# Performance work log

Measured on AMD Instinct MI355X. Metric: run time of the kernel, lower is better.

The kernel has to match this reference:

```python
import jax, jax.numpy as jnp
import numpy as np

B, SQ, SK, D_MODEL, H, D = 2, 2048, 2048, 1024, 16, 64


def setup_inputs() -> dict:
    key = jax.random.key(0)
    ks = jax.random.split(key, 10)
    s = 1.0 / np.sqrt(D_MODEL)
    return {
        "x": jax.random.normal(ks[0], (B, SK, D_MODEL), jnp.float32),
        "x2": jax.random.normal(ks[1], (B, SQ, D_MODEL), jnp.float32),
        "Wq": jax.random.normal(ks[2], (H, D_MODEL, D), jnp.float32) * s,
        "bq": jax.random.normal(ks[3], (H, D), jnp.float32) * s,
        "Wk": jax.random.normal(ks[4], (H, D_MODEL, D), jnp.float32) * s,
        "bk": jax.random.normal(ks[5], (H, D), jnp.float32) * s,
        "Wv": jax.random.normal(ks[6], (H, D_MODEL, D), jnp.float32) * s,
        "bv": jax.random.normal(ks[7], (H, D), jnp.float32) * s,
        "Wo": jax.random.normal(ks[8], (D_MODEL, D_MODEL), jnp.float32) * s,
        "bo": jax.random.normal(ks[9], (D_MODEL,), jnp.float32) * s,
    }


def reference(x, x2, Wq, bq, Wk, bk, Wv, bv, Wo, bo):
    # Batched per-head projections (fuses the Python per-head loop).
    # q: [B, H, SQ, D]; k,v: [B, H, SK, D]
    q = jnp.einsum("bsm,hmd->bhsd", x2, Wq) + bq[None, :, None, :]
    k = jnp.einsum("bsm,hmd->bhsd", x, Wk) + bk[None, :, None, :]
    v = jnp.einsum("bsm,hmd->bhsd", x, Wv) + bv[None, :, None, :]
    scale = 1.0 / jnp.sqrt(jnp.asarray(D, q.dtype))
    scores = jnp.einsum("bhqd,bhkd->bhqk", q, k) * scale  # [B,H,SQ,SK]
    attn = jax.nn.softmax(scores, axis=-1)
    o = jnp.einsum("bhqk,bhkd->bhqd", attn, v)  # [B,H,SQ,D]
    # concat heads along feature dim (head-major order matches torch.cat)
    o = o.transpose(0, 2, 1, 3).reshape(B, SQ, H * D)
    # final projection; dropout is identity in eval mode
    return o @ Wo.T + bo
```

## Files before the change

### kernel.cpp

```cpp
#include <hip/hip_runtime.h>
#include <math.h>

#define B_   2
#define SQ_  2048
#define SK_  2048
#define DM_  1024
#define H_   16
#define D_   64

typedef __attribute__((ext_vector_type(8))) short bf16x8;
typedef __attribute__((ext_vector_type(4))) float f32x4;
typedef unsigned int u32;

__device__ __forceinline__ short f2bf(float f) {
    union { float f; unsigned u; } v; v.f = f;
    unsigned r = v.u + 0x7FFFu + ((v.u >> 16) & 1u);
    return (short)(r >> 16);
}
__device__ __forceinline__ u32 pk2bf(float x, float y) {
    union { float f; u32 u; } a, b; a.f = x; b.f = y;
    return ((a.u + 0x8000u) >> 16) | ((b.u + 0x8000u) & 0xFFFF0000u);
}
__device__ __forceinline__ u32 pkbf_rh(float x, float y) {
    union { float f; u32 u; } a, b; a.f = x; b.f = y;
    return __builtin_amdgcn_perm(b.u + 0x8000u, a.u + 0x8000u, 0x07060302u);
}

__device__ __forceinline__ void gll16(const void* g, void* l) {
    __builtin_amdgcn_global_load_lds(
        (const __attribute__((address_space(1))) u32*)g,
        (__attribute__((address_space(3))) u32*)l, 16, 0, 0);
}

__global__ __launch_bounds__(256) void prep_kernel(
    const float* __restrict__ Wq, const float* __restrict__ Wk,
    const float* __restrict__ Wv, const float* __restrict__ Wo,
    const float* __restrict__ x,  const float* __restrict__ x2,
    short* __restrict__ WqT, short* __restrict__ WkT,
    short* __restrict__ WvT, short* __restrict__ Wob,
    short* __restrict__ xb,  short* __restrict__ x2b)
{
    const int t = threadIdx.x;
    const int z = blockIdx.z;
    if (z >= 3) {
        const float* src = (z == 3) ? Wo : (z == 4) ? x : x2;
        short* dst       = (z == 3) ? Wob : (z == 4) ? xb : x2b;
        int nloop = (z == 3) ? 4 : 16;
        int bid = blockIdx.y * 16 + blockIdx.x;
        #pragma unroll 4
        for (int j = 0; j < nloop; j++) {
            int i = bid * (nloop * 256) + j * 256 + t;
            float4 v = ((const float4*)src)[i];
            short4 s;
            s.x = f2bf(v.x); s.y = f2bf(v.y); s.z = f2bf(v.z); s.w = f2bf(v.w);
            ((short4*)dst)[i] = s;
        }
        return;
    }
    const float* W = (z == 0) ? Wq : (z == 1) ? Wk : Wv;
    short* WT      = (z == 0) ? WqT : (z == 1) ? WkT : WvT;
    const int h  = blockIdx.y;
    const int m0 = blockIdx.x * 64;
    __shared__ short Ls[64][68];

    #pragma unroll
    for (int it = 0; it < 4; it++) {
        int lin = it * 256 + t;
        int m = lin >> 4, d4 = lin & 15;
        float4 v = *(const float4*)&W[((long)h * DM_ + m0 + m) * D_ + d4 * 4];
        short4 s;
        s.x = f2bf(v.x); s.y = f2bf(v.y); s.z = f2bf(v.z); s.w = f2bf(v.w);
        *(short4*)&Ls[m][d4 * 4] = s;
    }
    __syncthreads();
    #pragma unroll
    for (int it = 0; it < 2; it++) {
        int d = (t >> 3) + it * 32, scol = t & 7;
        bf16x8 vv;
        #pragma unroll
        for (int j = 0; j < 8; j++) vv[j] = Ls[scol * 8 + j][d];
        *(bf16x8*)&WT[((long)h * 64 + d) * DM_ + m0 + scol * 8] = vv;
    }
}

__device__ __forceinline__ void gemm_stage(
    short* __restrict__ Asb, short* __restrict__ Bsb,
    const short* __restrict__ A, const short* __restrict__ Bw,
    int r0, int n0, int k0c, int w, int srow, int sc)
{
    #pragma unroll
    for (int j = 0; j < 4; j++) {
        int q   = w * 4 + j;
        int row = q * 8 + srow;
        gll16(A  + ((long)(r0 + row) << 10) + k0c + sc * 8, Asb + q * 512);
        gll16(Bw + ((long)(n0 + row) << 10) + k0c + sc * 8, Bsb + q * 512);
    }
}

template <int MODE>
__device__ __forceinline__ void gemm_core(
    short* __restrict__ Ls,
    const short* __restrict__ A, const short* __restrict__ Bw,
    const float* __restrict__ bias, void* __restrict__ outp,
    int r0, int n0, float oscale)
{
    const int t    = threadIdx.x;
    const int w    = t >> 6;
    const int ln   = t & 63;
    const int l15  = ln & 15;
    const int quad = ln >> 4;
    const int wr   = w >> 1;
    const int wc   = w & 1;

    f32x4 acc[4][4];
    #pragma unroll
    for (int i = 0; i < 4; i++)
        #pragma unroll
        for (int j = 0; j < 4; j++) acc[i][j] = (f32x4){0.f, 0.f, 0.f, 0.f};

    const int srow = ln >> 3;
    const int sc   = (ln & 7) ^ srow;
    const int rsw  = l15 & 7;

    gemm_stage(Ls, Ls + 8192, A, Bw, r0, n0, 0, w, srow, sc);

    int cur = 0;
    for (int k0 = 0; k0 < 1024; k0 += 64) {
        __syncthreads();
        if (k0 + 64 < 1024) {
            short* Anx = Ls + (cur ^ 1) * 16384;
            gemm_stage(Anx, Anx + 8192, A, Bw, r0, n0, k0 + 64, w, srow, sc);
        }
        const short* Asb = Ls + cur * 16384;
        const short* Bsb = Asb + 8192;
        #pragma unroll
        for (int kh = 0; kh < 2; kh++) {
            bf16x8 af[4], bfr[4];
            #pragma unroll
            for (int i = 0; i < 4; i++) {
                int ra = wr * 64 + i * 16 + l15;
                int rb = wc * 64 + i * 16 + l15;
                int pc = ((kh * 4 + quad) ^ rsw) * 8;
                af[i]  = *(const bf16x8*)&Asb[ra * 64 + pc];
                bfr[i] = *(const bf16x8*)&Bsb[rb * 64 + pc];
            }
            #pragma unroll
            for (int i = 0; i < 4; i++)
                #pragma unroll
                for (int j = 0; j < 4; j++)
                    acc[i][j] = __builtin_amdgcn_mfma_f32_16x16x32_bf16(
                        af[i], bfr[j], acc[i][j], 0, 0, 0);
        }
        cur ^= 1;
    }

    #pragma unroll
    for (int j = 0; j < 4; j++) {
        int col = n0 + wc * 64 + j * 16 + l15;
        float bv = bias[col];
        if (MODE == 2) {
            int hh = col >> 6, dd = col & 63;
            #pragma unroll
            for (int i = 0; i < 4; i++) {
                int rowb = r0 + wr * 64 + i * 16 + quad * 4;
                int bb = rowb >> 11, ss = rowb & 2047;
                int sl = ss & 63;
                int sp = (ss & ~63) | (sl & 35) | ((sl & 12) << 1) | ((sl & 16) >> 2);
                short4 sv;
                sv.x = f2bf(acc[i][j][0] + bv);
                sv.y = f2bf(acc[i][j][1] + bv);
                sv.z = f2bf(acc[i][j][2] + bv);
                sv.w = f2bf(acc[i][j][3] + bv);
                *(short4*)&((short*)outp)[
                    ((long)(((bb << 4) + hh) * 64 + dd) << 11) + sp] = sv;
            }
        } else {
            #pragma unroll
            for (int i = 0; i < 4; i++) {
                int rowb = r0 + wr * 64 + i * 16 + quad * 4;
                #pragma unroll
                for (int r = 0; r < 4; r++) {
                    float v = (acc[i][j][r] + bv) * oscale;
                    if (MODE == 0)
                        ((short*)outp)[(long)(rowb + r) * 1024 + col] = f2bf(v);
                    else
                        ((float*)outp)[(long)(rowb + r) * 1024 + col] = v;
                }
            }
        }
    }
}

#define QSCALE 0.180336880977f

__global__ __launch_bounds__(256) void gemm_qkv_kernel(
    const short* __restrict__ x2b, const short* __restrict__ xb,
    const short* __restrict__ WqT, const short* __restrict__ WkT,
    const short* __restrict__ WvT,
    const float* __restrict__ bq, const float* __restrict__ bk,
    const float* __restrict__ bv,
    short* __restrict__ Qb, short* __restrict__ Kb, short* __restrict__ VT)
{
    __shared__ short Ls[2 * 16384];
    const int z = blockIdx.z;
    if (z == 0) {
        gemm_core<0>(Ls, x2b, WqT, bq, Qb, blockIdx.x * 128, blockIdx.y * 128, QSCALE);
    } else if (z == 1) {
        gemm_core<0>(Ls, xb, WkT, bk, Kb, blockIdx.x * 128, blockIdx.y * 128, 1.0f);
    } else {
        gemm_core<2>(Ls, xb, WvT, bv, VT, blockIdx.x * 128, blockIdx.y * 128, 1.0f);
    }
}

__device__ __forceinline__ void gout_stage(
    short* __restrict__ Asb, short* __restrict__ Bsb,
    const short* __restrict__ A, const short* __restrict__ Bw,
    int r0, int n0, int k0c, int w, int srow, int sc)
{
    #pragma unroll
    for (int j = 0; j < 6; j++) {
        int q = w * 6 + j;
        if (q < 8) {
            int row = q * 8 + srow;
            gll16(A + ((long)(r0 + row) << 10) + k0c + sc * 8, Asb + q * 512);
        } else {
            int qb = q - 8;
            int row = qb * 8 + srow;
            gll16(Bw + ((long)(n0 + row) << 10) + k0c + sc * 8, Bsb + qb * 512);
        }
    }
}

__global__ __launch_bounds__(256) void gemm_out_kernel(
    const short* __restrict__ A, const short* __restrict__ Bw,
    const float* __restrict__ bias, float* __restrict__ outp)
{
    __shared__ short Ls[2 * 12288];

    const int r0   = blockIdx.x * 64;
    const int n0   = blockIdx.y * 128;
    const int t    = threadIdx.x;
    const int w    = t >> 6;
    const int ln   = t & 63;
    const int l15  = ln & 15;
    const int quad = ln >> 4;
    const int wr   = w >> 1;
    const int wc   = w & 1;

    f32x4 acc[2][4];
    #pragma unroll
    for (int i = 0; i < 2; i++)
        #pragma unroll
        for (int j = 0; j < 4; j++) acc[i][j] = (f32x4){0.f, 0.f, 0.f, 0.f};

    const int srow = ln >> 3;
    const int sc   = (ln & 7) ^ srow;
    const int rsw  = l15 & 7;

    gout_stage(Ls, Ls + 4096, A, Bw, r0, n0, 0, w, srow, sc);

    int cur = 0;
    for (int k0 = 0; k0 < 1024; k0 += 64) {
        __syncthreads();
        if (k0 + 64 < 1024) {
            short* Anx = Ls + (cur ^ 1) * 12288;
            gout_stage(Anx, Anx + 4096, A, Bw, r0, n0, k0 + 64, w, srow, sc);
        }
        const short* Asb = Ls + cur * 12288;
        const short* Bsb = Asb + 4096;
        #pragma unroll
        for (int kh = 0; kh < 2; kh++) {
            int pc = ((kh * 4 + quad) ^ rsw) * 8;
            bf16x8 af[2], bfr[4];
            #pragma unroll
            for (int i = 0; i < 2; i++)
                af[i] = *(const bf16x8*)&Asb[(wr * 32 + i * 16 + l15) * 64 + pc];
            #pragma unroll
            for (int j = 0; j < 4; j++)
                bfr[j] = *(const bf16x8*)&Bsb[(wc * 64 + j * 16 + l15) * 64 + pc];
            #pragma unroll
            for (int i = 0; i < 2; i++)
                #pragma unroll
                for (int j = 0; j < 4; j++)
                    acc[i][j] = __builtin_amdgcn_mfma_f32_16x16x32_bf16(
                        af[i], bfr[j], acc[i][j], 0, 0, 0);
        }
        cur ^= 1;
    }

    #pragma unroll
    for (int j = 0; j < 4; j++) {
        int col = n0 + wc * 64 + j * 16 + l15;
        float bv = bias[col];
        #pragma unroll
        for (int i = 0; i < 2; i++) {
            int rowb = r0 + wr * 32 + i * 16 + quad * 4;
            #pragma unroll
            for (int r = 0; r < 4; r++)
                outp[(long)(rowb + r) * 1024 + col] = acc[i][j][r] + bv;
        }
    }
}

__global__ __launch_bounds__(256, 2) void flash_kernel(
    const short* __restrict__ Q, const short* __restrict__ K,
    const short* __restrict__ VT, short* __restrict__ O)
{
    const int t    = threadIdx.x;
    const int wave = t >> 6;
    const int ln   = t & 63;
    const int l15  = ln & 15;
    const int quad = ln >> 4;
    const int f   = blockIdx.x + (blockIdx.y << 4);
    const int wid = ((f & 7) << 6) | (f >> 3);
    const int bh  = wid >> 4;
    const int b   = bh >> 4;
    const int h   = bh & 15;
    const int q0  = (wid & 15) * 128;
    const int wq  = q0 + wave * 32;

    __shared__ short Ks[2][2][64 * 64];
    __shared__ short Vs[2][2][64 * 64];

    const int srow = ln >> 3;
    const int sc   = (ln & 7) ^ srow;
    const int rsw  = l15 & 7;
    const int pc0  = ((quad    ) ^ rsw) * 8;
    const int pc1  = ((quad + 4) ^ rsw) * 8;
    const int rb   = l15 * 64;

    bf16x8 aQ0[2], aQ1[2];
    #pragma unroll
    for (int qg = 0; qg < 2; qg++) {
        const short* Qp = Q + ((long)(b * SQ_ + wq + qg * 16 + l15)) * 1024
                            + h * 64 + quad * 8;
        aQ0[qg] = *(const bf16x8*)(Qp);
        aQ1[qg] = *(const bf16x8*)(Qp + 32);
    }

    bf16x8 ones;
    #pragma unroll
    for (int j = 0; j < 8; j++) ones[j] = (short)0x3F80;

    const f32x4 fz = (f32x4){0.f, 0.f, 0.f, 0.f};

    f32x4 o_acc[2][4];
    f32x4 l_acc[2];
    #pragma unroll
    for (int qg = 0; qg < 2; qg++) {
        l_acc[qg] = fz;
        #pragma unroll
        for (int i = 0; i < 4; i++) o_acc[qg][i] = fz;
    }

    const short* Kbase = K  + ((long)b * SK_) * 1024 + h * 64;
    const short* Vbase = VT + (long)bh * D_ * SK_;
    const int qqa = wave * 2, qqb = wave * 2 + 1;
    const int rowa = qqa * 8 + srow, rowb_ = qqb * 8 + srow;

    #define STAGE(bufp, half, kbase)                                            \
        gll16(Kbase + (long)((kbase) + rowa)  * 1024 + sc * 8,                  \
              &Ks[bufp][half][qqa * 512]);                                      \
        gll16(Kbase + (long)((kbase) + rowb_) * 1024 + sc * 8,                  \
              &Ks[bufp][half][qqb * 512]);                                      \
        gll16(Vbase + (long)rowa  * 2048 + (kbase) + sc * 8,                    \
              &Vs[bufp][half][qqa * 512]);                                      \
        gll16(Vbase + (long)rowb_ * 2048 + (kbase) + sc * 8,                    \
              &Vs[bufp][half][qqb * 512]);

    STAGE(0, 0, 0)
    STAGE(0, 1, 64)

    u32 pwB[2][8];
    bf16x8 vfB[8];

    int cur = 0;
    for (int k0 = 0; k0 < SK_; k0 += 128) {
        __syncthreads();
        if (k0 + 128 < SK_) {
            int nx = cur ^ 1;
            STAGE(nx, 0, k0 + 128)
            STAGE(nx, 1, k0 + 192)
        }
        const short* K0 = &Ks[cur][0][0];
        const short* K1 = &Ks[cur][1][0];
        const short* V0 = &Vs[cur][0][0];
        const short* V1 = &Vs[cur][1][0];

        bf16x8 kfA[8];
        #pragma unroll
        for (int kt = 0; kt < 4; kt++) {
            const short* kr = &K0[kt * 1024 + rb];
            kfA[kt * 2    ] = *(const bf16x8*)&kr[pc0];
            kfA[kt * 2 + 1] = *(const bf16x8*)&kr[pc1];
        }

        if (k0) {
            bf16x8 aP0B[2], aP1B[2];
            #pragma unroll
            for (int qg = 0; qg < 2; qg++) {
                union { bf16x8 v; u32 w[4]; } u0, u1;
                u0.w[0] = pwB[qg][0]; u0.w[1] = pwB[qg][1];
                u0.w[2] = pwB[qg][2]; u0.w[3] = pwB[qg][3];
                u1.w[0] = pwB[qg][4]; u1.w[1] = pwB[qg][5];
                u1.w[2] = pwB[qg][6]; u1.w[3] = pwB[qg][7];
                aP0B[qg] = u0.v; aP1B[qg] = u1.v;
            }
            __builtin_amdgcn_s_setprio(1);
            #pragma unroll
            for (int qg = 0; qg < 2; qg++) {
                l_acc[qg] = __builtin_amdgcn_mfma_f32_16x16x32_bf16(aP0B[qg], ones, l_acc[qg], 0, 0, 0);
                l_acc[qg] = __builtin_amdgcn_mfma_f32_16x16x32_bf16(aP1B[qg], ones, l_acc[qg], 0, 0, 0);
            }
            #pragma unroll
            for (int dt = 0; dt < 4; dt++) {
                #pragma unroll
                for (int qg = 0; qg < 2; qg++) {
                    o_acc[qg][dt] = __builtin_amdgcn_mfma_f32_16x16x32_bf16(aP0B[qg], vfB[dt * 2    ], o_acc[qg][dt], 0, 0, 0);
                    o_acc[qg][dt] = __builtin_amdgcn_mfma_f32_16x16x32_bf16(aP1B[qg], vfB[dt * 2 + 1], o_acc[qg][dt], 0, 0, 0);
                }
            }
            __builtin_amdgcn_s_setprio(0);
        }

        bf16x8 kfB[8];
        #pragma unroll
        for (int kt = 0; kt < 4; kt++) {
            const short* kr = &K1[kt * 1024 + rb];
            kfB[kt * 2    ] = *(const bf16x8*)&kr[pc0];
            kfB[kt * 2 + 1] = *(const bf16x8*)&kr[pc1];
        }
        f32x4 zA[2][4], zB[2][4];
        #pragma unroll
        for (int kt = 0; kt < 4; kt++)
            #pragma unroll
            for (int qg = 0; qg < 2; qg++) {
                f32x4 z = __builtin_amdgcn_mfma_f32_16x16x32_bf16(kfA[kt * 2], aQ0[qg], fz, 0, 0, 0);
                zA[qg][kt] = __builtin_amdgcn_mfma_f32_16x16x32_bf16(kfA[kt * 2 + 1], aQ1[qg], z, 0, 0, 0);
            }

        bf16x8 vfA[8];
        #pragma unroll
        for (int dt = 0; dt < 4; dt++) {
            const short* vr = &V0[dt * 1024 + rb];
            vfA[dt * 2    ] = *(const bf16x8*)&vr[pc0];
            vfA[dt * 2 + 1] = *(const bf16x8*)&vr[pc1];
        }
        u32 pwA[2][8];
        #pragma unroll
        for (int kt = 0; kt < 4; kt++) {
            #pragma unroll
            for (int qg = 0; qg < 2; qg++) {
                f32x4 z = __builtin_amdgcn_mfma_f32_16x16x32_bf16(kfB[kt * 2], aQ0[qg], fz, 0, 0, 0);
                zB[qg][kt] = __builtin_amdgcn_mfma_f32_16x16x32_bf16(kfB[kt * 2 + 1], aQ1[qg], z, 0, 0, 0);
            }
            #pragma unroll
            for (int qg = 0; qg < 2; qg++) {
                f32x4 s = zA[qg][kt];
                pwA[qg][kt * 2    ] = pkbf_rh(__builtin_amdgcn_exp2f(s[0]),
                                              __builtin_amdgcn_exp2f(s[1]));
                pwA[qg][kt * 2 + 1] = pkbf_rh(__builtin_amdgcn_exp2f(s[2]),
                                              __builtin_amdgcn_exp2f(s[3]));
            }
        }

        bf16x8 aP0A[2], aP1A[2];
        #pragma unroll
        for (int qg = 0; qg < 2; qg++) {
            union { bf16x8 v; u32 w[4]; } u0, u1;
            u0.w[0] = pwA[qg][0]; u0.w[1] = pwA[qg][1];
            u0.w[2] = pwA[qg][2]; u0.w[3] = pwA[qg][3];
            u1.w[0] = pwA[qg][4]; u1.w[1] = pwA[qg][5];
            u1.w[2] = pwA[qg][6]; u1.w[3] = pwA[qg][7];
            aP0A[qg] = u0.v; aP1A[qg] = u1.v;
            l_acc[qg] = __builtin_amdgcn_mfma_f32_16x16x32_bf16(aP0A[qg], ones, l_acc[qg], 0, 0, 0);
            l_acc[qg] = __builtin_amdgcn_mfma_f32_16x16x32_bf16(aP1A[qg], ones, l_acc[qg], 0, 0, 0);
        }

        #pragma unroll
        for (int dt = 0; dt < 4; dt++) {
            const short* vr = &V1[dt * 1024 + rb];
            vfB[dt * 2    ] = *(const bf16x8*)&vr[pc0];
            vfB[dt * 2 + 1] = *(const bf16x8*)&vr[pc1];
        }
        #pragma unroll
        for (int dt = 0; dt < 4; dt++) {
            #pragma unroll
            for (int qg = 0; qg < 2; qg++) {
                o_acc[qg][dt] = __builtin_amdgcn_mfma_f32_16x16x32_bf16(aP0A[qg], vfA[dt * 2    ], o_acc[qg][dt], 0, 0, 0);
                o_acc[qg][dt] = __builtin_amdgcn_mfma_f32_16x16x32_bf16(aP1A[qg], vfA[dt * 2 + 1], o_acc[qg][dt], 0, 0, 0);
            }
            #pragma unroll
            for (int qg = 0; qg < 2; qg++) {
                f32x4 s = zB[qg][dt];
                pwB[qg][dt * 2    ] = pkbf_rh(__builtin_amdgcn_exp2f(s[0]),
                                              __builtin_amdgcn_exp2f(s[1]));
                pwB[qg][dt * 2 + 1] = pkbf_rh(__builtin_amdgcn_exp2f(s[2]),
                                              __builtin_amdgcn_exp2f(s[3]));
            }
        }
        cur ^= 1;
    }
    #undef STAGE

    {
        bf16x8 aP0B[2], aP1B[2];
        #pragma unroll
        for (int qg = 0; qg < 2; qg++) {
            union { bf16x8 v; u32 w[4]; } u0, u1;
            u0.w[0] = pwB[qg][0]; u0.w[1] = pwB[qg][1];
            u0.w[2] = pwB[qg][2]; u0.w[3] = pwB[qg][3];
            u1.w[0] = pwB[qg][4]; u1.w[1] = pwB[qg][5];
            u1.w[2] = pwB[qg][6]; u1.w[3] = pwB[qg][7];
            aP0B[qg] = u0.v; aP1B[qg] = u1.v;
            l_acc[qg] = __builtin_amdgcn_mfma_f32_16x16x32_bf16(aP0B[qg], ones, l_acc[qg], 0, 0, 0);
            l_acc[qg] = __builtin_amdgcn_mfma_f32_16x16x32_bf16(aP1B[qg], ones, l_acc[qg], 0, 0, 0);
        }
        #pragma unroll
        for (int dt = 0; dt < 4; dt++) {
            #pragma unroll
            for (int qg = 0; qg < 2; qg++) {
                o_acc[qg][dt] = __builtin_amdgcn_mfma_f32_16x16x32_bf16(aP0B[qg], vfB[dt * 2    ], o_acc[qg][dt], 0, 0, 0);
                o_acc[qg][dt] = __builtin_amdgcn_mfma_f32_16x16x32_bf16(aP1B[qg], vfB[dt * 2 + 1], o_acc[qg][dt], 0, 0, 0);
            }
        }
    }

    #pragma unroll
    for (int qg = 0; qg < 2; qg++) {
        #pragma unroll
        for (int r = 0; r < 4; r++) {
            float inv = 1.0f / l_acc[qg][r];
            long row = (long)b * SQ_ + wq + qg * 16 + quad * 4 + r;
            short* Op = O + row * 1024 + h * 64 + l15;
            #pragma unroll
            for (int dt = 0; dt < 4; dt++)
                Op[dt * 16] = f2bf(o_acc[qg][dt][r] * inv);
        }
    }
}

extern "C" void kernel_launch(void* const* d_in, const int* in_sizes, int n_in,
                              void* d_out, int out_size, void* d_ws, size_t ws_size,
                              hipStream_t stream) {
    const float* x  = (const float*)d_in[0];
    const float* x2 = (const float*)d_in[1];
    const float* Wq = (const float*)d_in[2];
    const float* bq = (const float*)d_in[3];
    const float* Wk = (const float*)d_in[4];
    const float* bk = (const float*)d_in[5];
    const float* Wv = (const float*)d_in[6];
    const float* bv = (const float*)d_in[7];
    const float* Wo = (const float*)d_in[8];
    const float* bo = (const float*)d_in[9];
    float* out = (float*)d_out;

    const size_t nAct = (size_t)B_ * SK_ * DM_;
    const size_t nW   = (size_t)DM_ * DM_;
    short* bufA = (short*)d_ws;
    short* bufB = bufA + nAct;
    short* Qb   = bufB + nAct;
    short* Kb   = Qb + nAct;
    short* VTws = Kb + nAct;
    short* WqT  = VTws + nAct;
    short* WkT  = WqT + nW;
    short* WvT  = WkT + nW;
    short* Wob  = WvT + nW;

    prep_kernel<<<dim3(16, 16, 6), 256, 0, stream>>>(
        Wq, Wk, Wv, Wo, x, x2, WqT, WkT, WvT, Wob, bufA, bufB);

    gemm_qkv_kernel<<<dim3(32, 8, 3), 256, 0, stream>>>(
        bufB, bufA, WqT, WkT, WvT, bq, bk, bv, Qb, Kb, VTws);

    flash_kernel<<<dim3(16, 32), 256, 0, stream>>>(Qb, Kb, VTws, bufB);
    gemm_out_kernel<<<dim3(64, 8), 256, 0, stream>>>(bufB, Wob, bo, out);
}
```

Before: 190.3 us.

## Give each flash-attention wave 64 query rows with 2-wave blocks

Each flash kernel block now uses 2 waves (128 threads) instead of 4, and each wave processes 64 query rows (4 groups of 16) instead of 32. Every K/V fragment read from LDS is therefore reused across twice as many query rows, which lowers LDS read traffic per MFMA, and staging is split across fewer waves with four loads each. The cost is much higher register pressure from doubled accumulators, score tiles and P words. With launch bounds of 1 block per CU that could cut occupancy or cause spills, and fewer waves remain to hide latency.

```diff
diff --git a/kernel.cpp b/kernel.cpp
--- a/kernel.cpp
+++ b/kernel.cpp
@@ -302,7 +302,8 @@
     }
 }
 
-__global__ __launch_bounds__(256, 2) void flash_kernel(
+#define QG 4
+__global__ __launch_bounds__(128, 1) void flash_kernel(
     const short* __restrict__ Q, const short* __restrict__ K,
     const short* __restrict__ VT, short* __restrict__ O)
 {
@@ -317,7 +318,7 @@
     const int b   = bh >> 4;
     const int h   = bh & 15;
     const int q0  = (wid & 15) * 128;
-    const int wq  = q0 + wave * 32;
+    const int wq  = q0 + wave * 64;
 
     __shared__ short Ks[2][2][64 * 64];
     __shared__ short Vs[2][2][64 * 64];
@@ -329,9 +330,9 @@
     const int pc1  = ((quad + 4) ^ rsw) * 8;
     const int rb   = l15 * 64;
 
-    bf16x8 aQ0[2], aQ1[2];
-    #pragma unroll
-    for (int qg = 0; qg < 2; qg++) {
+    bf16x8 aQ0[QG], aQ1[QG];
+    #pragma unroll
+    for (int qg = 0; qg < QG; qg++) {
         const short* Qp = Q + ((long)(b * SQ_ + wq + qg * 16 + l15)) * 1024
                             + h * 64 + quad * 8;
         aQ0[qg] = *(const bf16x8*)(Qp);
@@ -344,10 +345,10 @@
 
     const f32x4 fz = (f32x4){0.f, 0.f, 0.f, 0.f};
 
-    f32x4 o_acc[2][4];
-    f32x4 l_acc[2];
-    #pragma unroll
-    for (int qg = 0; qg < 2; qg++) {
+    f32x4 o_acc[QG][4];
+    f32x4 l_acc[QG];
+    #pragma unroll
+    for (int qg = 0; qg < QG; qg++) {
         l_acc[qg] = fz;
         #pragma unroll
         for (int i = 0; i < 4; i++) o_acc[qg][i] = fz;
@@ -355,23 +356,22 @@
 
     const short* Kbase = K  + ((long)b * SK_) * 1024 + h * 64;
     const short* Vbase = VT + (long)bh * D_ * SK_;
-    const int qqa = wave * 2, qqb = wave * 2 + 1;
-    const int rowa = qqa * 8 + srow, rowb_ = qqb * 8 + srow;
 
     #define STAGE(bufp, half, kbase)                                            \
-        gll16(Kbase + (long)((kbase) + rowa)  * 1024 + sc * 8,                  \
-              &Ks[bufp][half][qqa * 512]);                                      \
-        gll16(Kbase + (long)((kbase) + rowb_) * 1024 + sc * 8,                  \
-              &Ks[bufp][half][qqb * 512]);                                      \
-        gll16(Vbase + (long)rowa  * 2048 + (kbase) + sc * 8,                    \
-              &Vs[bufp][half][qqa * 512]);                                      \
-        gll16(Vbase + (long)rowb_ * 2048 + (kbase) + sc * 8,                    \
-              &Vs[bufp][half][qqb * 512]);
+        _Pragma("unroll")                                                       \
+        for (int j_ = 0; j_ < 4; j_++) {                                        \
+            int qq_  = wave * 4 + j_;                                           \
+            int row_ = qq_ * 8 + srow;                                          \
+            gll16(Kbase + (long)((kbase) + row_) * 1024 + sc * 8,               \
+                  &Ks[bufp][half][qq_ * 512]);                                  \
+            gll16(Vbase + (long)row_ * 2048 + (kbase) + sc * 8,                 \
+                  &Vs[bufp][half][qq_ * 512]);                                  \
+        }
 
     STAGE(0, 0, 0)
     STAGE(0, 1, 64)
 
-    u32 pwB[2][8];
+    u32 pwB[QG][8];
     bf16x8 vfB[8];
 
     int cur = 0;
@@ -396,28 +396,20 @@
         }
 
         if (k0) {
-            bf16x8 aP0B[2], aP1B[2];
-            #pragma unroll
-            for (int qg = 0; qg < 2; qg++) {
+            __builtin_amdgcn_s_setprio(1);
+            #pragma unroll
+            for (int qg = 0; qg < QG; qg++) {
                 union { bf16x8 v; u32 w[4]; } u0, u1;
                 u0.w[0] = pwB[qg][0]; u0.w[1] = pwB[qg][1];
                 u0.w[2] = pwB[qg][2]; u0.w[3] = pwB[qg][3];
                 u1.w[0] = pwB[qg][4]; u1.w[1] = pwB[qg][5];
                 u1.w[2] = pwB[qg][6]; u1.w[3] = pwB[qg][7];
-                aP0B[qg] = u0.v; aP1B[qg] = u1.v;
-            }
-            __builtin_amdgcn_s_setprio(1);
-            #pragma unroll
-            for (int qg = 0; qg < 2; qg++) {
-                l_acc[qg] = __builtin_amdgcn_mfma_f32_16x16x32_bf16(aP0B[qg], ones, l_acc[qg], 0, 0, 0);
-                l_acc[qg] = __builtin_amdgcn_mfma_f32_16x16x32_bf16(aP1B[qg], ones, l_acc[qg], 0, 0, 0);
-            }
-            #pragma unroll
-            for (int dt = 0; dt < 4; dt++) {
+                l_acc[qg] = __builtin_amdgcn_mfma_f32_16x16x32_bf16(u0.v, ones, l_acc[qg], 0, 0, 0);
+                l_acc[qg] = __builtin_amdgcn_mfma_f32_16x16x32_bf16(u1.v, ones, l_acc[qg], 0, 0, 0);
                 #pragma unroll
-                for (int qg = 0; qg < 2; qg++) {
-                    o_acc[qg][dt] = __builtin_amdgcn_mfma_f32_16x16x32_bf16(aP0B[qg], vfB[dt * 2    ], o_acc[qg][dt], 0, 0, 0);
-                    o_acc[qg][dt] = __builtin_amdgcn_mfma_f32_16x16x32_bf16(aP1B[qg], vfB[dt * 2 + 1], o_acc[qg][dt], 0, 0, 0);
+                for (int dt = 0; dt < 4; dt++) {
+                    o_acc[qg][dt] = __builtin_amdgcn_mfma_f32_16x16x32_bf16(u0.v, vfB[dt * 2    ], o_acc[qg][dt], 0, 0, 0);
+                    o_acc[qg][dt] = __builtin_amdgcn_mfma_f32_16x16x32_bf16(u1.v, vfB[dt * 2 + 1], o_acc[qg][dt], 0, 0, 0);
                 }
             }
             __builtin_amdgcn_s_setprio(0);
@@ -430,11 +422,11 @@
             kfB[kt * 2    ] = *(const bf16x8*)&kr[pc0];
             kfB[kt * 2 + 1] = *(const bf16x8*)&kr[pc1];
         }
-        f32x4 zA[2][4], zB[2][4];
+        f32x4 zA[QG][4], zB[QG][4];
         #pragma unroll
         for (int kt = 0; kt < 4; kt++)
             #pragma unroll
-            for (int qg = 0; qg < 2; qg++) {
+            for (int qg = 0; qg < QG; qg++) {
                 f32x4 z = __builtin_amdgcn_mfma_f32_16x16x32_bf16(kfA[kt * 2], aQ0[qg], fz, 0, 0, 0);
                 zA[qg][kt] = __builtin_amdgcn_mfma_f32_16x16x32_bf16(kfA[kt * 2 + 1], aQ1[qg], z, 0, 0, 0);
             }
@@ -446,16 +438,16 @@
             vfA[dt * 2    ] = *(const bf16x8*)&vr[pc0];
             vfA[dt * 2 + 1] = *(const bf16x8*)&vr[pc1];
         }
-        u32 pwA[2][8];
+        u32 pwA[QG][8];
         #pragma unroll
         for (int kt = 0; kt < 4; kt++) {
             #pragma unroll
-            for (int qg = 0; qg < 2; qg++) {
+            for (int qg = 0; qg < QG; qg++) {
                 f32x4 z = __builtin_amdgcn_mfma_f32_16x16x32_bf16(kfB[kt * 2], aQ0[qg], fz, 0, 0, 0);
                 zB[qg][kt] = __builtin_amdgcn_mfma_f32_16x16x32_bf16(kfB[kt * 2 + 1], aQ1[qg], z, 0, 0, 0);
             }
             #pragma unroll
-            for (int qg = 0; qg < 2; qg++) {
+            for (int qg = 0; qg < QG; qg++) {
                 f32x4 s = zA[qg][kt];
                 pwA[qg][kt * 2    ] = pkbf_rh(__builtin_amdgcn_exp2f(s[0]),
                                               __builtin_amdgcn_exp2f(s[1]));
@@ -464,9 +456,9 @@
             }
         }
 
-        bf16x8 aP0A[2], aP1A[2];
-        #pragma unroll
-        for (int qg = 0; qg < 2; qg++) {
+        bf16x8 aP0A[QG], aP1A[QG];
+        #pragma unroll
+        for (int qg = 0; qg < QG; qg++) {
             union { bf16x8 v; u32 w[4]; } u0, u1;
             u0.w[0] = pwA[qg][0]; u0.w[1] = pwA[qg][1];
             u0.w[2] = pwA[qg][2]; u0.w[3] = pwA[qg][3];
@@ -486,12 +478,12 @@
         #pragma unroll
         for (int dt = 0; dt < 4; dt++) {
             #pragma unroll
-            for (int qg = 0; qg < 2; qg++) {
+            for (int qg = 0; qg < QG; qg++) {
                 o_acc[qg][dt] = __builtin_amdgcn_mfma_f32_16x16x32_bf16(aP0A[qg], vfA[dt * 2    ], o_acc[qg][dt], 0, 0, 0);
                 o_acc[qg][dt] = __builtin_amdgcn_mfma_f32_16x16x32_bf16(aP1A[qg], vfA[dt * 2 + 1], o_acc[qg][dt], 0, 0, 0);
             }
             #pragma unroll
-            for (int qg = 0; qg < 2; qg++) {
+            for (int qg = 0; qg < QG; qg++) {
                 f32x4 s = zB[qg][dt];
                 pwB[qg][dt * 2    ] = pkbf_rh(__builtin_amdgcn_exp2f(s[0]),
                                               __builtin_amdgcn_exp2f(s[1]));
@@ -503,31 +495,24 @@
     }
     #undef STAGE
 
-    {
-        bf16x8 aP0B[2], aP1B[2];
-        #pragma unroll
-        for (int qg = 0; qg < 2; qg++) {
-            union { bf16x8 v; u32 w[4]; } u0, u1;
-            u0.w[0] = pwB[qg][0]; u0.w[1] = pwB[qg][1];
-            u0.w[2] = pwB[qg][2]; u0.w[3] = pwB[qg][3];
-            u1.w[0] = pwB[qg][4]; u1.w[1] = pwB[qg][5];
-            u1.w[2] = pwB[qg][6]; u1.w[3] = pwB[qg][7];
-            aP0B[qg] = u0.v; aP1B[qg] = u1.v;
-            l_acc[qg] = __builtin_amdgcn_mfma_f32_16x16x32_bf16(aP0B[qg], ones, l_acc[qg], 0, 0, 0);
-            l_acc[qg] = __builtin_amdgcn_mfma_f32_16x16x32_bf16(aP1B[qg], ones, l_acc[qg], 0, 0, 0);
-        }
+    #pragma unroll
+    for (int qg = 0; qg < QG; qg++) {
+        union { bf16x8 v; u32 w[4]; } u0, u1;
+        u0.w[0] = pwB[qg][0]; u0.w[1] = pwB[qg][1];
+        u0.w[2] = pwB[qg][2]; u0.w[3] = pwB[qg][3];
+        u1.w[0] = pwB[qg][4]; u1.w[1] = pwB[qg][5];
+        u1.w[2] = pwB[qg][6]; u1.w[3] = pwB[qg][7];
+        l_acc[qg] = __builtin_amdgcn_mfma_f32_16x16x32_bf16(u0.v, ones, l_acc[qg], 0, 0, 0);
+        l_acc[qg] = __builtin_amdgcn_mfma_f32_16x16x32_bf16(u1.v, ones, l_acc[qg], 0, 0, 0);
         #pragma unroll
         for (int dt = 0; dt < 4; dt++) {
-            #pragma unroll
-            for (int qg = 0; qg < 2; qg++) {
-                o_acc[qg][dt] = __builtin_amdgcn_mfma_f32_16x16x32_bf16(aP0B[qg], vfB[dt * 2    ], o_acc[qg][dt], 0, 0, 0);
-                o_acc[qg][dt] = __builtin_amdgcn_mfma_f32_16x16x32_bf16(aP1B[qg], vfB[dt * 2 + 1], o_acc[qg][dt], 0, 0, 0);
-            }
-        }
-    }
-
-    #pragma unroll
-    for (int qg = 0; qg < 2; qg++) {
+            o_acc[qg][dt] = __builtin_amdgcn_mfma_f32_16x16x32_bf16(u0.v, vfB[dt * 2    ], o_acc[qg][dt], 0, 0, 0);
+            o_acc[qg][dt] = __builtin_amdgcn_mfma_f32_16x16x32_bf16(u1.v, vfB[dt * 2 + 1], o_acc[qg][dt], 0, 0, 0);
+        }
+    }
+
+    #pragma unroll
+    for (int qg = 0; qg < QG; qg++) {
         #pragma unroll
         for (int r = 0; r < 4; r++) {
             float inv = 1.0f / l_acc[qg][r];
@@ -573,6 +558,6 @@
     gemm_qkv_kernel<<<dim3(32, 8, 3), 256, 0, stream>>>(
         bufB, bufA, WqT, WkT, WvT, bq, bk, bv, Qb, Kb, VTws);
 
-    flash_kernel<<<dim3(16, 32), 256, 0, stream>>>(Qb, Kb, VTws, bufB);
+    flash_kernel<<<dim3(16, 32), 128, 0, stream>>>(Qb, Kb, VTws, bufB);
     gemm_out_kernel<<<dim3(64, 8), 256, 0, stream>>>(bufB, Wob, bo, out);
 }
```

New measurement: 203.9 us. 7.2% more time.

## Shrink flash attention blocks to two waves and single 64-key tiles

Applied to the files above, without the earlier changes.

The flash kernel now runs 128-thread blocks of two waves covering 64 query rows, with twice as many blocks. Each iteration stages and processes one 64-key tile instead of two half-tiles, which shrinks shared memory per block and drops the intra-iteration software pipelining between the A and B halves. More, smaller blocks aim to raise occupancy and spread work across CUs, but each K/V tile is reused by fewer waves, so global/L2 traffic per query rises and there are twice as many barriers per key.

```diff
diff --git a/kernel.cpp b/kernel.cpp
--- a/kernel.cpp
+++ b/kernel.cpp
@@ -302,7 +302,7 @@
     }
 }
 
-__global__ __launch_bounds__(256, 2) void flash_kernel(
+__global__ __launch_bounds__(128, 2) void flash_kernel(
     const short* __restrict__ Q, const short* __restrict__ K,
     const short* __restrict__ VT, short* __restrict__ O)
 {
@@ -311,16 +311,16 @@
     const int ln   = t & 63;
     const int l15  = ln & 15;
     const int quad = ln >> 4;
-    const int f   = blockIdx.x + (blockIdx.y << 4);
-    const int wid = ((f & 7) << 6) | (f >> 3);
-    const int bh  = wid >> 4;
+    const int f   = blockIdx.x + (blockIdx.y << 5);
+    const int wid = ((f & 7) << 7) | (f >> 3);
+    const int bh  = wid >> 5;
     const int b   = bh >> 4;
     const int h   = bh & 15;
-    const int q0  = (wid & 15) * 128;
+    const int q0  = (wid & 31) * 64;
     const int wq  = q0 + wave * 32;
 
-    __shared__ short Ks[2][2][64 * 64];
-    __shared__ short Vs[2][2][64 * 64];
+    __shared__ short Ks[2][64 * 64];
+    __shared__ short Vs[2][64 * 64];
 
     const int srow = ln >> 3;
     const int sc   = (ln & 7) ^ srow;
@@ -355,44 +355,38 @@
 
     const short* Kbase = K  + ((long)b * SK_) * 1024 + h * 64;
     const short* Vbase = VT + (long)bh * D_ * SK_;
-    const int qqa = wave * 2, qqb = wave * 2 + 1;
-    const int rowa = qqa * 8 + srow, rowb_ = qqb * 8 + srow;
-
-    #define STAGE(bufp, half, kbase)                                            \
-        gll16(Kbase + (long)((kbase) + rowa)  * 1024 + sc * 8,                  \
-              &Ks[bufp][half][qqa * 512]);                                      \
-        gll16(Kbase + (long)((kbase) + rowb_) * 1024 + sc * 8,                  \
-              &Ks[bufp][half][qqb * 512]);                                      \
-        gll16(Vbase + (long)rowa  * 2048 + (kbase) + sc * 8,                    \
-              &Vs[bufp][half][qqa * 512]);                                      \
-        gll16(Vbase + (long)rowb_ * 2048 + (kbase) + sc * 8,                    \
-              &Vs[bufp][half][qqb * 512]);
-
-    STAGE(0, 0, 0)
-    STAGE(0, 1, 64)
+
+    #define STAGE(bufp, kbase)                                                  \
+        _Pragma("unroll")                                                       \
+        for (int j_ = 0; j_ < 4; j_++) {                                        \
+            int qq_  = wave * 4 + j_;                                           \
+            int row_ = qq_ * 8 + srow;                                          \
+            gll16(Kbase + (long)((kbase) + row_) * 1024 + sc * 8,               \
+                  &Ks[bufp][qq_ * 512]);                                        \
+            gll16(Vbase + (long)row_ * 2048 + (kbase) + sc * 8,                 \
+                  &Vs[bufp][qq_ * 512]);                                        \
+        }
+
+    STAGE(0, 0)
 
     u32 pwB[2][8];
     bf16x8 vfB[8];
 
     int cur = 0;
-    for (int k0 = 0; k0 < SK_; k0 += 128) {
+    for (int k0 = 0; k0 < SK_; k0 += 64) {
         __syncthreads();
-        if (k0 + 128 < SK_) {
-            int nx = cur ^ 1;
-            STAGE(nx, 0, k0 + 128)
-            STAGE(nx, 1, k0 + 192)
-        }
-        const short* K0 = &Ks[cur][0][0];
-        const short* K1 = &Ks[cur][1][0];
-        const short* V0 = &Vs[cur][0][0];
-        const short* V1 = &Vs[cur][1][0];
-
-        bf16x8 kfA[8];
+        if (k0 + 64 < SK_) {
+            STAGE(cur ^ 1, k0 + 64)
+        }
+        const short* K0 = &Ks[cur][0];
+        const short* V0 = &Vs[cur][0];
+
+        bf16x8 kf[8];
         #pragma unroll
         for (int kt = 0; kt < 4; kt++) {
             const short* kr = &K0[kt * 1024 + rb];
-            kfA[kt * 2    ] = *(const bf16x8*)&kr[pc0];
-            kfA[kt * 2 + 1] = *(const bf16x8*)&kr[pc1];
+            kf[kt * 2    ] = *(const bf16x8*)&kr[pc0];
+            kf[kt * 2 + 1] = *(const bf16x8*)&kr[pc1];
         }
 
         if (k0) {
@@ -423,82 +417,33 @@
             __builtin_amdgcn_s_setprio(0);
         }
 
-        bf16x8 kfB[8];
-        #pragma unroll
-        for (int kt = 0; kt < 4; kt++) {
-            const short* kr = &K1[kt * 1024 + rb];
-            kfB[kt * 2    ] = *(const bf16x8*)&kr[pc0];
-            kfB[kt * 2 + 1] = *(const bf16x8*)&kr[pc1];
-        }
-        f32x4 zA[2][4], zB[2][4];
+        f32x4 z[2][4];
         #pragma unroll
         for (int kt = 0; kt < 4; kt++)
             #pragma unroll
             for (int qg = 0; qg < 2; qg++) {
-                f32x4 z = __builtin_amdgcn_mfma_f32_16x16x32_bf16(kfA[kt * 2], aQ0[qg], fz, 0, 0, 0);
-                zA[qg][kt] = __builtin_amdgcn_mfma_f32_16x16x32_bf16(kfA[kt * 2 + 1], aQ1[qg], z, 0, 0, 0);
-            }
-
-        bf16x8 vfA[8];
+                f32x4 zz = __builtin_amdgcn_mfma_f32_16x16x32_bf16(kf[kt * 2], aQ0[qg], fz, 0, 0, 0);
+                z[qg][kt] = __builtin_amdgcn_mfma_f32_16x16x32_bf16(kf[kt * 2 + 1], aQ1[qg], zz, 0, 0, 0);
+            }
+
         #pragma unroll
         for (int dt = 0; dt < 4; dt++) {
             const short* vr = &V0[dt * 1024 + rb];
-            vfA[dt * 2    ] = *(const bf16x8*)&vr[pc0];
-            vfA[dt * 2 + 1] = *(const bf16x8*)&vr[pc1];
-        }
-        u32 pwA[2][8];
-        #pragma unroll
-        for (int kt = 0; kt < 4; kt++) {
-            #pragma unroll
-            for (int qg = 0; qg < 2; qg++) {
-                f32x4 z = __builtin_amdgcn_mfma_f32_16x16x32_bf16(kfB[kt * 2], aQ0[qg], fz, 0, 0, 0);
-                zB[qg][kt] = __builtin_amdgcn_mfma_f32_16x16x32_bf16(kfB[kt * 2 + 1], aQ1[qg], z, 0, 0, 0);
-            }
-            #pragma unroll
-            for (int qg = 0; qg < 2; qg++) {
-                f32x4 s = zA[qg][kt];
-                pwA[qg][kt * 2    ] = pkbf_rh(__builtin_amdgcn_exp2f(s[0]),
-                                              __builtin_amdgcn_exp2f(s[1]));
-                pwA[qg][kt * 2 + 1] = pkbf_rh(__builtin_amdgcn_exp2f(s[2]),
-                                              __builtin_amdgcn_exp2f(s[3]));
-            }
-        }
-
-        bf16x8 aP0A[2], aP1A[2];
-        #pragma unroll
-        for (int qg = 0; qg < 2; qg++) {
-            union { bf16x8 v; u32 w[4]; } u0, u1;
-            u0.w[0] = pwA[qg][0]; u0.w[1] = pwA[qg][1];
-            u0.w[2] = pwA[qg][2]; u0.w[3] = pwA[qg][3];
-            u1.w[0] = pwA[qg][4]; u1.w[1] = pwA[qg][5];
-            u1.w[2] = pwA[qg][6]; u1.w[3] = pwA[qg][7];
-            aP0A[qg] = u0.v; aP1A[qg] = u1.v;
-            l_acc[qg] = __builtin_amdgcn_mfma_f32_16x16x32_bf16(aP0A[qg], ones, l_acc[qg], 0, 0, 0);
-            l_acc[qg] = __builtin_amdgcn_mfma_f32_16x16x32_bf16(aP1A[qg], ones, l_acc[qg], 0, 0, 0);
-        }
-
-        #pragma unroll
-        for (int dt = 0; dt < 4; dt++) {
-            const short* vr = &V1[dt * 1024 + rb];
             vfB[dt * 2    ] = *(const bf16x8*)&vr[pc0];
             vfB[dt * 2 + 1] = *(const bf16x8*)&vr[pc1];
         }
-        #pragma unroll
-        for (int dt = 0; dt < 4; dt++) {
+
+        #pragma unroll
+        for (int kt = 0; kt < 4; kt++)
             #pragma unroll
             for (int qg = 0; qg < 2; qg++) {
-                o_acc[qg][dt] = __builtin_amdgcn_mfma_f32_16x16x32_bf16(aP0A[qg], vfA[dt * 2    ], o_acc[qg][dt], 0, 0, 0);
-                o_acc[qg][dt] = __builtin_amdgcn_mfma_f32_16x16x32_bf16(aP1A[qg], vfA[dt * 2 + 1], o_acc[qg][dt], 0, 0, 0);
-            }
-            #pragma unroll
-            for (int qg = 0; qg < 2; qg++) {
-                f32x4 s = zB[qg][dt];
-                pwB[qg][dt * 2    ] = pkbf_rh(__builtin_amdgcn_exp2f(s[0]),
+                f32x4 s = z[qg][kt];
+                pwB[qg][kt * 2    ] = pkbf_rh(__builtin_amdgcn_exp2f(s[0]),
                                               __builtin_amdgcn_exp2f(s[1]));
-                pwB[qg][dt * 2 + 1] = pkbf_rh(__builtin_amdgcn_exp2f(s[2]),
+                pwB[qg][kt * 2 + 1] = pkbf_rh(__builtin_amdgcn_exp2f(s[2]),
                                               __builtin_amdgcn_exp2f(s[3]));
             }
-        }
+
         cur ^= 1;
     }
     #undef STAGE
@@ -573,6 +518,6 @@
     gemm_qkv_kernel<<<dim3(32, 8, 3), 256, 0, stream>>>(
         bufB, bufA, WqT, WkT, WvT, bq, bk, bv, Qb, Kb, VTws);
 
-    flash_kernel<<<dim3(16, 32), 256, 0, stream>>>(Qb, Kb, VTws, bufB);
+    flash_kernel<<<dim3(32, 32), 128, 0, stream>>>(Qb, Kb, VTws, bufB);
     gemm_out_kernel<<<dim3(64, 8), 256, 0, stream>>>(bufB, Wob, bo, out);
 }
```

After: 195.0 us. +2.5%, slower.
